# Kernel tuning notes

Measured on AMD Instinct MI355X. Metric: run time of the kernel, lower is better.

## Reference

```python
import jax, jax.numpy as jnp
import numpy as np

B, T, D = 4, 2048, 2048
DI = int(D * 2.0)  # mlp_expansion = 2.0
RMS_EPS = 1e-6
LRU_EPS = 1e-6
INIT_SCALE = 0.02


def _rmsnorm(x, w):
    return x * jax.lax.rsqrt(jnp.mean(x * x, axis=-1, keepdims=True) + RMS_EPS) * w


def setup_inputs() -> dict:
    key = jax.random.key(0)
    ks = jax.random.split(key, 10)
    s = INIT_SCALE
    return {
        "x": jax.random.normal(ks[0], (B, T, D), dtype=jnp.float32),
        "state": jnp.zeros((B, D), dtype=jnp.float32),
        "w_norm1": jnp.ones((D,), dtype=jnp.float32),
        "W_in": jax.random.normal(ks[1], (D, D), dtype=jnp.float32) * s,
        "W_r": jax.random.normal(ks[2], (D, D), dtype=jnp.float32) * s,
        "b_r": jnp.zeros((D,), dtype=jnp.float32),
        "W_i": jax.random.normal(ks[3], (D, D), dtype=jnp.float32) * s,
        "b_i": jnp.zeros((D,), dtype=jnp.float32),
        "log_decay": jax.random.normal(ks[4], (D,), dtype=jnp.float32),
        "W_out": jax.random.normal(ks[5], (D, D), dtype=jnp.float32) * s,
        "w_norm2": jnp.ones((D,), dtype=jnp.float32),
        "W_gate": jax.random.normal(ks[6], (DI, D), dtype=jnp.float32) * s,
        "W_up": jax.random.normal(ks[7], (DI, D), dtype=jnp.float32) * s,
        "W_down": jax.random.normal(ks[8], (D, DI), dtype=jnp.float32) * s,
    }


def reference(x, state, w_norm1, W_in, W_r, b_r, W_i, b_i, log_decay,
              W_out, w_norm2, W_gate, W_up, W_down):
    # --- pre-norm + RG-LRU mixer ---
    n = _rmsnorm(x, w_norm1)                      # (B,T,D)
    r = jax.nn.sigmoid(n @ W_r.T + b_r)           # input gate
    g = jax.nn.sigmoid(n @ W_i.T + b_i)           # recurrent gate
    xp = n @ W_in.T                               # projected input
    alpha = jnp.clip(jax.nn.sigmoid(log_decay), LRU_EPS, 1.0 - LRU_EPS)  # (D,)
    scale = jnp.sqrt(jnp.clip(1.0 - alpha * alpha, 0.0, None))           # (D,)
    b_seq = scale * (r * xp)                      # (B,T,D)

    def step(h, b_t):                             # h_t = alpha*h + scale*(r_t*x_t)
        h = alpha * h + b_t
        return h, h

    h_final, hs = jax.lax.scan(step, state, jnp.swapaxes(b_seq, 0, 1))  # hs: (T,B,D)
    hs = jnp.swapaxes(hs, 0, 1)                   # (B,T,D)
    mixer_out = (hs * g) @ W_out.T
    x = x + mixer_out

    # --- SwiGLU FFN ---
    n2 = _rmsnorm(x, w_norm2)
    ffn = (jax.nn.silu(n2 @ W_gate.T) * (n2 @ W_up.T)) @ W_down.T
    return x + ffn, h_final
```

## Files before the change

### kernel.cpp

```cpp
#include <hip/hip_runtime.h>

#define BD 4
#define TD 2048
#define DD 2048
#define DID 4096
#define MD (BD*TD)
#define CHK 32
#define CHL (TD/CHK)

typedef float f32x4 __attribute__((ext_vector_type(4)));
typedef short s16x8 __attribute__((ext_vector_type(8)));
typedef unsigned short u16;
typedef unsigned short u16x4 __attribute__((ext_vector_type(4)));
typedef unsigned short u16x8 __attribute__((ext_vector_type(8)));

__device__ __forceinline__ float bf2f(u16 u) {
    union { unsigned int i; float f; } v; v.i = ((unsigned int)u) << 16; return v.f;
}
__device__ __forceinline__ u16 f2bf(float f) {
    union { float f; unsigned int i; } v; v.f = f;
    unsigned int r = v.i + 0x7fffu + ((v.i >> 16) & 1u);
    return (u16)(r >> 16);
}
__device__ __forceinline__ float sigm(float x) { return 1.f / (1.f + __expf(-x)); }

__device__ __forceinline__ void mfma16(f32x4& acc, s16x8 a, s16x8 b) {
    asm("v_mfma_f32_16x16x32_bf16 %0, %1, %2, %0" : "+v"(acc) : "v"(a), "v"(b));
}

__device__ __forceinline__ void gload16(const u16* g, u16* l) {
    __builtin_amdgcn_global_load_lds((__attribute__((address_space(1))) void*)(g),
                                     (__attribute__((address_space(3))) void*)(l),
                                     16, 0, 0);
}

__global__ __launch_bounds__(256)
void cvt_all(const float4* __restrict__ sr, const float4* __restrict__ sin_,
             const float4* __restrict__ si, const float4* __restrict__ sout,
             const float4* __restrict__ sg, const float4* __restrict__ su,
             const float4* __restrict__ sd, u16x4* __restrict__ dst, int n4) {
    const int SEG  = DD * DD / 4;
    const int ROWQ = DD / 4;
    int i = blockIdx.x * blockDim.x + threadIdx.x;
    int stride = gridDim.x * blockDim.x;
    for (; i < n4; i += stride) {
        const float4* s; int off; size_t di;
        if (i < 2 * SEG) {
            int which = i / SEG;
            int jj = i - which * SEG;
            int g = jj / ROWQ, cq = jj - g * ROWQ;
            int nb = g >> 6, ii = g & 63;
            int dr = which == 0 ? nb * 128 + (ii < 32 ? ii : ii + 32)
                                : nb * 128 + (ii < 32 ? ii + 32 : ii + 64);
            s = which ? sin_ : sr; off = jj;
            di = (size_t)dr * ROWQ + cq;
        } else if (i < 3 * SEG) {
            s = si; off = i - 2 * SEG; di = i;
        } else if (i < 4 * SEG) {
            s = sout; off = i - 3 * SEG; di = i;
        } else if (i < 8 * SEG) {
            int j = i - 4 * SEG;
            int which = j / (2 * SEG);
            int jj = j - which * 2 * SEG;
            int g = jj / ROWQ, cq = jj - g * ROWQ;
            int nb = g >> 6, ii = g & 63;
            int dr = which == 0 ? nb * 128 + (ii < 32 ? ii : ii + 32)
                                : nb * 128 + (ii < 32 ? ii + 32 : ii + 64);
            s = which ? su : sg; off = jj;
            di = (size_t)4 * SEG + (size_t)dr * ROWQ + cq;
        } else {
            s = sd; off = i - 8 * SEG; di = i;
        }
        float4 v = s[off];
        u16x4 o = { f2bf(v.x), f2bf(v.y), f2bf(v.z), f2bf(v.w) };
        dst[di] = o;
    }
}

__global__ __launch_bounds__(256) void rmsnorm_kernel(const float* __restrict__ x,
                                                      const float* __restrict__ w,
                                                      u16* __restrict__ out) {
    const int row = blockIdx.x;
    const int tid = threadIdx.x;
    const float4* x4 = (const float4*)(x + (size_t)row * DD);
    float4 a = x4[tid * 2], b = x4[tid * 2 + 1];
    float s = a.x*a.x + a.y*a.y + a.z*a.z + a.w*a.w
            + b.x*b.x + b.y*b.y + b.z*b.z + b.w*b.w;
#pragma unroll
    for (int off = 32; off >= 1; off >>= 1) s += __shfl_xor(s, off, 64);
    __shared__ float red[4];
    if ((tid & 63) == 0) red[tid >> 6] = s;
    __syncthreads();
    float tot = red[0] + red[1] + red[2] + red[3];
    float rs = rsqrtf(tot * (1.f / DD) + 1e-6f);
    const float4* w4 = (const float4*)w;
    float4 wa = w4[tid * 2], wb = w4[tid * 2 + 1];
    u16x8 o = { f2bf(a.x*rs*wa.x), f2bf(a.y*rs*wa.y), f2bf(a.z*rs*wa.z), f2bf(a.w*rs*wa.w),
                f2bf(b.x*rs*wb.x), f2bf(b.y*rs*wb.y), f2bf(b.z*rs*wb.z), f2bf(b.w*rs*wb.w) };
    *(u16x8*)(out + (size_t)row * DD + tid * 8) = o;
}

template<int EPI>
__global__ __launch_bounds__(256)
void gemm_bt(const u16* __restrict__ A, const u16* __restrict__ Bw,
             int M, int N, int K,
             const float* __restrict__ bias0, const float* __restrict__ bias1,
             const float* resid, float* outf,
             u16* __restrict__ out0, u16* __restrict__ out1, int Dsub) {
    __shared__ __align__(16) u16 lA[128 * 64];
    __shared__ __align__(16) u16 lB[128 * 64];
    const int tid  = threadIdx.x;
    const int lane = tid & 63;
    const int wave = tid >> 6;
    const int wr = (wave >> 1) << 6;
    const int wc = (wave & 1) << 6;
    const int brow = blockIdx.x * 128;
    const int bcol = blockIdx.y * 128;

    const int srow  = tid >> 3;
    const int schnk = (tid & 7) ^ (srow & 7);
    const size_t soff = (size_t)srow * K + (schnk << 3);
    const u16* gA = A  + (size_t)brow * K + soff;
    const u16* gB = Bw + (size_t)bcol * K + soff;
    u16* lAp = lA + tid * 8;
    u16* lBp = lB + tid * 8;

    const int fr = lane & 15;
    const int lg = lane >> 4;
    const int ck0 = ((lg)     ^ (fr & 7)) << 4;
    const int ck1 = ((4 + lg) ^ (fr & 7)) << 4;
    const char* lAc = (const char*)lA;
    const char* lBc = (const char*)lB;

    f32x4 acc[4][4];
#pragma unroll
    for (int i = 0; i < 4; ++i)
#pragma unroll
        for (int j = 0; j < 4; ++j)
            acc[i][j] = (f32x4){0.f, 0.f, 0.f, 0.f};

    for (int k0 = 0; k0 < K; k0 += 64) {
#pragma unroll
        for (int s = 0; s < 4; ++s) {
            gload16(gA + k0 + (size_t)s * 32 * K, lAp + s * 2048);
            gload16(gB + k0 + (size_t)s * 32 * K, lBp + s * 2048);
        }
        __syncthreads();
        s16x8 af[4][2], bq[4][2];
#pragma unroll
        for (int i = 0; i < 4; ++i) {
            const int ra = (wr + i * 16 + fr) * 128;
            const int rb = (wc + i * 16 + fr) * 128;
            af[i][0] = *(const s16x8*)(lAc + ra + ck0);
            af[i][1] = *(const s16x8*)(lAc + ra + ck1);
            bq[i][0] = *(const s16x8*)(lBc + rb + ck0);
            bq[i][1] = *(const s16x8*)(lBc + rb + ck1);
        }
#pragma unroll
        for (int h = 0; h < 2; ++h)
#pragma unroll
            for (int i = 0; i < 4; ++i)
#pragma unroll
                for (int j = 0; j < 4; ++j)
                    mfma16(acc[i][j], af[i][h], bq[j][h]);
        __syncthreads();
    }

#pragma unroll
    for (int i = 0; i < 4; ++i)
#pragma unroll
        for (int j = 0; j < 4; ++j)
            asm volatile("s_nop 7" : "+v"(acc[i][j]));

    const int r0 = brow + wr + (lg << 2);

    if (EPI == 3 || (EPI == 6 && bcol < 2 * DD)) {
        const int nb = bcol >> 7;
        const int cbase = nb * 64 + (wc ? 32 : 0);
#pragma unroll
        for (int i = 0; i < 4; ++i)
#pragma unroll
            for (int j = 0; j < 2; ++j)
#pragma unroll
                for (int e = 0; e < 4; ++e) {
                    const int grow = r0 + i * 16 + e;
                    const int col  = cbase + j * 16 + fr;
                    const float g = acc[i][j][e];
                    const float u = acc[i][j + 2][e];
                    float v;
                    if (EPI == 3) v = g * sigm(g) * u;
                    else          v = sigm(g + bias0[col]) * u;
                    out0[(size_t)grow * Dsub + col] = f2bf(v);
                }
        return;
    }

    const int c0 = bcol + wc + fr;
#pragma unroll
    for (int i = 0; i < 4; ++i) {
#pragma unroll
        for (int j = 0; j < 4; ++j) {
            const int gcol = c0 + j * 16;
#pragma unroll
            for (int e = 0; e < 4; ++e) {
                const int grow = r0 + i * 16 + e;
                float c = acc[i][j][e];
                if (EPI == 1) {
                    const size_t idx = (size_t)grow * N + gcol;
                    outf[idx] = resid[idx] + c;
                } else {
                    const int gc = gcol - 2 * DD;
                    out1[(size_t)grow * Dsub + gc] = f2bf(sigm(c + bias1[gc]));
                }
            }
        }
    }
}

__global__ __launch_bounds__(256)
void scan_partial(const u16x4* __restrict__ BP4,
                  const float4* __restrict__ ld4, float4* __restrict__ carry4) {
    const int d4 = blockIdx.x * 256 + threadIdx.x;
    const int k = blockIdx.y;
    const int b = blockIdx.z;
    const float4 ld = ld4[d4];
    float a[4], sc[4], h[4];
#pragma unroll
    for (int c = 0; c < 4; ++c) {
        float av = sigm(((const float*)&ld)[c]);
        av = fminf(fmaxf(av, 1e-6f), 1.f - 1e-6f);
        a[c] = av; sc[c] = sqrtf(fmaxf(1.f - av * av, 0.f)); h[c] = 0.f;
    }
    size_t idx = (((size_t)b * TD + (size_t)k * CHL) * DD >> 2) + d4;
#pragma unroll 8
    for (int t = 0; t < CHL; ++t) {
        u16x4 bp = BP4[idx];
#pragma unroll
        for (int c = 0; c < 4; ++c) h[c] = a[c] * h[c] + sc[c] * bf2f(bp[c]);
        idx += DD >> 2;
    }
    float4 o = { h[0], h[1], h[2], h[3] };
    carry4[(((size_t)b * CHK + k) * DD >> 2) + d4] = o;
}

__global__ __launch_bounds__(256)
void scan_final(const u16x4* __restrict__ BP4, const u16x4* __restrict__ G4,
                const float4* __restrict__ ld4, const float4* __restrict__ state4,
                const float4* __restrict__ carry4,
                u16x4* __restrict__ HSG4, float4* __restrict__ hfin4) {
    const int d4 = blockIdx.x * 256 + threadIdx.x;
    const int k = blockIdx.y;
    const int b = blockIdx.z;
    const float4 ld = ld4[d4];
    float a[4], sc[4], aL[4], h[4];
    const float4 st = state4[((size_t)b * DD >> 2) + d4];
#pragma unroll
    for (int c = 0; c < 4; ++c) {
        float av = sigm(((const float*)&ld)[c]);
        av = fminf(fmaxf(av, 1e-6f), 1.f - 1e-6f);
        a[c] = av; sc[c] = sqrtf(fmaxf(1.f - av * av, 0.f));
        float p = av;
#pragma unroll
        for (int i = 0; i < 6; ++i) p *= p;
        aL[c] = p;
        h[c] = ((const float*)&st)[c];
    }
    for (int kk = 0; kk < k; ++kk) {
        float4 cv = carry4[(((size_t)b * CHK + kk) * DD >> 2) + d4];
#pragma unroll
        for (int c = 0; c < 4; ++c) h[c] = aL[c] * h[c] + ((const float*)&cv)[c];
    }
    size_t idx = (((size_t)b * TD + (size_t)k * CHL) * DD >> 2) + d4;
#pragma unroll 8
    for (int t = 0; t < CHL; ++t) {
        u16x4 bp = BP4[idx];
        u16x4 gv = G4[idx];
        u16x4 o;
#pragma unroll
        for (int c = 0; c < 4; ++c) {
            h[c] = a[c] * h[c] + sc[c] * bf2f(bp[c]);
            o[c] = f2bf(h[c] * bf2f(gv[c]));
        }
        HSG4[idx] = o;
        idx += DD >> 2;
    }
    if (k == CHK - 1) {
        float4 o = { h[0], h[1], h[2], h[3] };
        hfin4[((size_t)b * DD >> 2) + d4] = o;
    }
}

extern "C" void kernel_launch(void* const* d_in, const int* in_sizes, int n_in,
                              void* d_out, int out_size, void* d_ws, size_t ws_size,
                              hipStream_t stream) {
    const float* x       = (const float*)d_in[0];
    const float* state   = (const float*)d_in[1];
    const float* w_norm1 = (const float*)d_in[2];
    const float* W_in    = (const float*)d_in[3];
    const float* W_r     = (const float*)d_in[4];
    const float* b_r     = (const float*)d_in[5];
    const float* W_i     = (const float*)d_in[6];
    const float* b_i     = (const float*)d_in[7];
    const float* log_dec = (const float*)d_in[8];
    const float* W_out   = (const float*)d_in[9];
    const float* w_norm2 = (const float*)d_in[10];
    const float* W_gate  = (const float*)d_in[11];
    const float* W_up    = (const float*)d_in[12];
    const float* W_down  = (const float*)d_in[13];

    float* out  = (float*)d_out;
    float* hfin = out + (size_t)MD * DD;

    const size_t SEGU = (size_t)DD * DD;
    u16* w_rx    = (u16*)d_ws;
    u16* w_out   = w_rx   + 3 * SEGU;
    u16* w_gu    = w_rx   + 4 * SEGU;
    u16* w_down  = w_rx   + 8 * SEGU;
    u16* bufN    = w_rx   + 10 * SEGU;
    u16* bufBP   = bufN   + (size_t)MD * DD;
    u16* bufG    = bufBP  + (size_t)MD * DD;
    u16* spare   = bufG   + (size_t)MD * DD;
    float* carry = (float*)spare;

    cvt_all<<<2048, 256, 0, stream>>>((const float4*)W_r, (const float4*)W_in,
                                      (const float4*)W_i, (const float4*)W_out,
                                      (const float4*)W_gate, (const float4*)W_up,
                                      (const float4*)W_down, (u16x4*)w_rx,
                                      (int)(10 * SEGU / 4));

    rmsnorm_kernel<<<MD, 256, 0, stream>>>(x, w_norm1, bufN);

    {
        dim3 g1(MD / 128, (3 * DD) / 128);
        gemm_bt<6><<<g1, 256, 0, stream>>>(bufN, w_rx, MD, 3 * DD, DD,
                                           b_r, b_i, nullptr, nullptr, bufBP, bufG, DD);
    }

    {
        dim3 gp(DD / 1024, CHK, BD);
        scan_partial<<<gp, 256, 0, stream>>>((const u16x4*)bufBP,
                                             (const float4*)log_dec, (float4*)carry);
        scan_final<<<gp, 256, 0, stream>>>((const u16x4*)bufBP, (const u16x4*)bufG,
                                           (const float4*)log_dec, (const float4*)state,
                                           (const float4*)carry,
                                           (u16x4*)bufN, (float4*)hfin);
    }

    {
        dim3 g2(MD / 128, DD / 128);
        gemm_bt<1><<<g2, 256, 0, stream>>>(bufN, w_out, MD, DD, DD,
                                           nullptr, nullptr, x, out, nullptr, nullptr, 0);
    }

    rmsnorm_kernel<<<MD, 256, 0, stream>>>(out, w_norm2, bufN);

    {
        dim3 g3(MD / 128, (2 * DID) / 128);
        gemm_bt<3><<<g3, 256, 0, stream>>>(bufN, w_gu, MD, 2 * DID, DD,
                                           nullptr, nullptr, nullptr, nullptr, bufBP, nullptr, DID);
    }

    {
        dim3 g4(MD / 128, DD / 128);
        gemm_bt<1><<<g4, 256, 0, stream>>>(bufBP, w_down, MD, DD, DID,
                                           nullptr, nullptr, out, out, nullptr, nullptr, 0);
    }
}
```

Before: 819.5 us.

## Store mid-residual in bf16 and hoist chunk-carry propagation into dedicated kernel

Result: faster. 773.8 us (-5.6%).

```diff
diff --git a/kernel.cpp b/kernel.cpp
--- a/kernel.cpp
+++ b/kernel.cpp
@@ -100,6 +100,30 @@
     *(u16x8*)(out + (size_t)row * DD + tid * 8) = o;
 }
 
+__global__ __launch_bounds__(256) void rmsnorm_bf16(const u16* __restrict__ x,
+                                                    const float* __restrict__ w,
+                                                    u16* __restrict__ out) {
+    const int row = blockIdx.x;
+    const int tid = threadIdx.x;
+    u16x8 v = *(const u16x8*)(x + (size_t)row * DD + tid * 8);
+    float f[8];
+    float s = 0.f;
+#pragma unroll
+    for (int c = 0; c < 8; ++c) { f[c] = bf2f(v[c]); s += f[c] * f[c]; }
+#pragma unroll
+    for (int off = 32; off >= 1; off >>= 1) s += __shfl_xor(s, off, 64);
+    __shared__ float red[4];
+    if ((tid & 63) == 0) red[tid >> 6] = s;
+    __syncthreads();
+    float tot = red[0] + red[1] + red[2] + red[3];
+    float rs = rsqrtf(tot * (1.f / DD) + 1e-6f);
+    const float4* w4 = (const float4*)w;
+    float4 wa = w4[tid * 2], wb = w4[tid * 2 + 1];
+    u16x8 o = { f2bf(f[0]*rs*wa.x), f2bf(f[1]*rs*wa.y), f2bf(f[2]*rs*wa.z), f2bf(f[3]*rs*wa.w),
+                f2bf(f[4]*rs*wb.x), f2bf(f[5]*rs*wb.y), f2bf(f[6]*rs*wb.z), f2bf(f[7]*rs*wb.w) };
+    *(u16x8*)(out + (size_t)row * DD + tid * 8) = o;
+}
+
 template<int EPI>
 __global__ __launch_bounds__(256)
 void gemm_bt(const u16* __restrict__ A, const u16* __restrict__ Bw,
@@ -205,9 +229,12 @@
             for (int e = 0; e < 4; ++e) {
                 const int grow = r0 + i * 16 + e;
                 float c = acc[i][j][e];
-                if (EPI == 1) {
+                if (EPI == 7) {
                     const size_t idx = (size_t)grow * N + gcol;
-                    outf[idx] = resid[idx] + c;
+                    out0[idx] = f2bf(resid[idx] + c);
+                } else if (EPI == 8) {
+                    const size_t idx = (size_t)grow * N + gcol;
+                    outf[idx] = bf2f(out1[idx]) + c;
                 } else {
                     const int gc = gcol - 2 * DD;
                     out1[(size_t)grow * Dsub + gc] = f2bf(sigm(c + bias1[gc]));
@@ -244,31 +271,53 @@
 }
 
 __global__ __launch_bounds__(256)
+void scan_carry(const float4* __restrict__ state4, const float4* __restrict__ ld4,
+                const float4* __restrict__ carry4, float4* __restrict__ carryin4,
+                float4* __restrict__ hfin4) {
+    const int d4 = blockIdx.x * 256 + threadIdx.x;
+    const int b = blockIdx.y;
+    const float4 ld = ld4[d4];
+    float aL[4], h[4];
+    const float4 st = state4[((size_t)b * DD >> 2) + d4];
+#pragma unroll
+    for (int c = 0; c < 4; ++c) {
+        float av = sigm(((const float*)&ld)[c]);
+        av = fminf(fmaxf(av, 1e-6f), 1.f - 1e-6f);
+        float p = av;
+#pragma unroll
+        for (int i = 0; i < 6; ++i) p *= p;
+        aL[c] = p;
+        h[c] = ((const float*)&st)[c];
+    }
+#pragma unroll
+    for (int k = 0; k < CHK; ++k) {
+        const size_t ci = (((size_t)b * CHK + k) * DD >> 2) + d4;
+        float4 o = { h[0], h[1], h[2], h[3] };
+        carryin4[ci] = o;
+        float4 cv = carry4[ci];
+#pragma unroll
+        for (int c = 0; c < 4; ++c) h[c] = aL[c] * h[c] + ((const float*)&cv)[c];
+    }
+    float4 o = { h[0], h[1], h[2], h[3] };
+    hfin4[((size_t)b * DD >> 2) + d4] = o;
+}
+
+__global__ __launch_bounds__(256)
 void scan_final(const u16x4* __restrict__ BP4, const u16x4* __restrict__ G4,
-                const float4* __restrict__ ld4, const float4* __restrict__ state4,
-                const float4* __restrict__ carry4,
-                u16x4* __restrict__ HSG4, float4* __restrict__ hfin4) {
+                const float4* __restrict__ ld4, const float4* __restrict__ carryin4,
+                u16x4* __restrict__ HSG4) {
     const int d4 = blockIdx.x * 256 + threadIdx.x;
     const int k = blockIdx.y;
     const int b = blockIdx.z;
     const float4 ld = ld4[d4];
-    float a[4], sc[4], aL[4], h[4];
-    const float4 st = state4[((size_t)b * DD >> 2) + d4];
+    float a[4], sc[4], h[4];
+    const float4 ci = carryin4[(((size_t)b * CHK + k) * DD >> 2) + d4];
 #pragma unroll
     for (int c = 0; c < 4; ++c) {
         float av = sigm(((const float*)&ld)[c]);
         av = fminf(fmaxf(av, 1e-6f), 1.f - 1e-6f);
         a[c] = av; sc[c] = sqrtf(fmaxf(1.f - av * av, 0.f));
-        float p = av;
-#pragma unroll
-        for (int i = 0; i < 6; ++i) p *= p;
-        aL[c] = p;
-        h[c] = ((const float*)&st)[c];
-    }
-    for (int kk = 0; kk < k; ++kk) {
-        float4 cv = carry4[(((size_t)b * CHK + kk) * DD >> 2) + d4];
-#pragma unroll
-        for (int c = 0; c < 4; ++c) h[c] = aL[c] * h[c] + ((const float*)&cv)[c];
+        h[c] = ((const float*)&ci)[c];
     }
     size_t idx = (((size_t)b * TD + (size_t)k * CHL) * DD >> 2) + d4;
 #pragma unroll 8
@@ -283,10 +332,6 @@
         }
         HSG4[idx] = o;
         idx += DD >> 2;
-    }
-    if (k == CHK - 1) {
-        float4 o = { h[0], h[1], h[2], h[3] };
-        hfin4[((size_t)b * DD >> 2) + d4] = o;
     }
 }
 
@@ -319,8 +364,9 @@
     u16* bufN    = w_rx   + 10 * SEGU;
     u16* bufBP   = bufN   + (size_t)MD * DD;
     u16* bufG    = bufBP  + (size_t)MD * DD;
-    u16* spare   = bufG   + (size_t)MD * DD;
-    float* carry = (float*)spare;
+    u16* bufX2   = bufG   + (size_t)MD * DD;
+    float* carry   = (float*)(bufX2 + (size_t)MD * DD);
+    float* carryin = carry + (size_t)BD * CHK * DD;
 
     cvt_all<<<2048, 256, 0, stream>>>((const float4*)W_r, (const float4*)W_in,
                                       (const float4*)W_i, (const float4*)W_out,
@@ -340,19 +386,22 @@
         dim3 gp(DD / 1024, CHK, BD);
         scan_partial<<<gp, 256, 0, stream>>>((const u16x4*)bufBP,
                                              (const float4*)log_dec, (float4*)carry);
+        dim3 gc(DD / 1024, BD);
+        scan_carry<<<gc, 256, 0, stream>>>((const float4*)state, (const float4*)log_dec,
+                                           (const float4*)carry, (float4*)carryin,
+                                           (float4*)hfin);
         scan_final<<<gp, 256, 0, stream>>>((const u16x4*)bufBP, (const u16x4*)bufG,
-                                           (const float4*)log_dec, (const float4*)state,
-                                           (const float4*)carry,
-                                           (u16x4*)bufN, (float4*)hfin);
+                                           (const float4*)log_dec, (const float4*)carryin,
+                                           (u16x4*)bufN);
     }
 
     {
         dim3 g2(MD / 128, DD / 128);
-        gemm_bt<1><<<g2, 256, 0, stream>>>(bufN, w_out, MD, DD, DD,
-                                           nullptr, nullptr, x, out, nullptr, nullptr, 0);
-    }
-
-    rmsnorm_kernel<<<MD, 256, 0, stream>>>(out, w_norm2, bufN);
+        gemm_bt<7><<<g2, 256, 0, stream>>>(bufN, w_out, MD, DD, DD,
+                                           nullptr, nullptr, x, nullptr, bufX2, nullptr, 0);
+    }
+
+    rmsnorm_bf16<<<MD, 256, 0, stream>>>(bufX2, w_norm2, bufN);
 
     {
         dim3 g3(MD / 128, (2 * DID) / 128);
@@ -362,7 +411,7 @@
 
     {
         dim3 g4(MD / 128, DD / 128);
-        gemm_bt<1><<<g4, 256, 0, stream>>>(bufBP, w_down, MD, DD, DID,
-                                           nullptr, nullptr, out, out, nullptr, nullptr, 0);
-    }
-}
+        gemm_bt<8><<<g4, 256, 0, stream>>>(bufBP, w_down, MD, DD, DID,
+                                           nullptr, nullptr, nullptr, out, nullptr, bufX2, 0);
+    }
+}
```
